# Performance work log

Hardware: AMD Instinct MI355X
Metric: run time of the kernel (lower is better)

Reference implementation:

```python
import jax, jax.numpy as jnp
import numpy as np

EMBED = 1024
HEADS = 16
HEAD_DIM = EMBED // HEADS


def setup_inputs() -> dict:
    key = jax.random.key(0)
    ks = jax.random.split(key, 5)
    s = 1.0 / np.sqrt(EMBED)
    return {
        "x": jax.random.normal(ks[0], (4, 2048, EMBED), dtype=jnp.float32),
        "W_qkv": jax.random.uniform(ks[1], (EMBED, 3 * EMBED), jnp.float32, -s, s),
        "b_qkv": jax.random.uniform(ks[2], (3 * EMBED,), jnp.float32, -s, s),
        "W_out": jax.random.uniform(ks[3], (EMBED, EMBED), jnp.float32, -s, s),
        "b_out": jax.random.uniform(ks[4], (EMBED,), jnp.float32, -s, s),
    }


def reference(x, W_qkv, b_qkv, W_out, b_out):
    B, S, E = x.shape
    qkv = x @ W_qkv + b_qkv  # [B,S,3E]
    q, k, v = jnp.split(qkv, 3, axis=-1)
    # [B,S,E] -> [B,H,S,D]
    def split_heads(t):
        return t.reshape(B, S, HEADS, HEAD_DIM).transpose(0, 2, 1, 3)
    q, k, v = split_heads(q), split_heads(k), split_heads(v)
    scale = 1.0 / jnp.sqrt(jnp.asarray(HEAD_DIM, dtype=x.dtype))
    scores = jnp.einsum("bhqd,bhkd->bhqk", q, k) * scale
    attn = jax.nn.softmax(scores, axis=-1)
    out = jnp.einsum("bhqk,bhkd->bhqd", attn, v)
    out = out.transpose(0, 2, 1, 3).reshape(B, S, E)
    return out @ W_out + b_out
```

## Files before the change

kernel.cpp:

```cpp
#include <hip/hip_runtime.h>
#include <hip/hip_bf16.h>

typedef __bf16 bf16;
typedef __bf16 bf16x8 __attribute__((ext_vector_type(8)));
typedef float f32x4 __attribute__((ext_vector_type(4)));
typedef float f32x16 __attribute__((ext_vector_type(16)));

#define EMB 1024
#define SEQ 2048
#define NH 16
#define HD 64
#define MTOK 8192

__global__ __launch_bounds__(256) void cast_f32_bf16(const float* __restrict__ in,
                                                     bf16* __restrict__ out, int n8) {
    int i = blockIdx.x * blockDim.x + threadIdx.x;
    if (i < n8) {
        const float4* p = (const float4*)in + 2 * (size_t)i;
        float4 a = p[0], b = p[1];
        bf16x8 v;
        v[0] = (bf16)a.x; v[1] = (bf16)a.y; v[2] = (bf16)a.z; v[3] = (bf16)a.w;
        v[4] = (bf16)b.x; v[5] = (bf16)b.y; v[6] = (bf16)b.z; v[7] = (bf16)b.w;
        *(bf16x8*)(out + 8 * (size_t)i) = v;
    }
}

__global__ __launch_bounds__(256) void transpose_cast(const float* __restrict__ W,
                                                      bf16* __restrict__ Wt, int K, int N) {
    __shared__ float tile[32][33];
    int n0 = blockIdx.x * 32, k0 = blockIdx.y * 32;
    int tx = threadIdx.x & 31, ty = threadIdx.x >> 5;
    #pragma unroll
    for (int i = 0; i < 32; i += 8)
        tile[ty + i][tx] = W[(size_t)(k0 + ty + i) * N + n0 + tx];
    __syncthreads();
    #pragma unroll
    for (int i = 0; i < 32; i += 8)
        Wt[(size_t)(n0 + ty + i) * K + k0 + tx] = (bf16)tile[tx][ty + i];
}

#define BM 128
#define BN 128
#define BK 64
#define LDK 72

#define QSCALE 0.1803368801111f

__global__ __launch_bounds__(256) void gemm_qkv(const bf16* __restrict__ A,
                                                const bf16* __restrict__ Bt,
                                                const float* __restrict__ bias,
                                                bf16* __restrict__ qws, bf16* __restrict__ kws,
                                                bf16* __restrict__ vt) {
    __shared__ bf16 sA[BM][LDK];
    __shared__ bf16 sB[BN][LDK];
    const int K = 1024;
    int m0 = blockIdx.x * BM, n0 = blockIdx.y * BN;
    int t = threadIdx.x, lane = t & 63, w = t >> 6;
    int wr = w >> 1, wc = w & 1;
    int l15 = lane & 15, quad = lane >> 4;

    f32x4 acc[4][4];
    #pragma unroll
    for (int i = 0; i < 4; i++)
        #pragma unroll
        for (int j = 0; j < 4; j++) acc[i][j] = (f32x4){0.f, 0.f, 0.f, 0.f};

    int srow = t >> 3, sc8 = (t & 7) * 8;
    for (int kt = 0; kt < K; kt += BK) {
        #pragma unroll
        for (int p = 0; p < 4; p++) {
            int r = srow + p * 32;
            *(uint4*)&sA[r][sc8] = *(const uint4*)(A + (size_t)(m0 + r) * K + kt + sc8);
            *(uint4*)&sB[r][sc8] = *(const uint4*)(Bt + (size_t)(n0 + r) * K + kt + sc8);
        }
        __syncthreads();
        #pragma unroll
        for (int ks = 0; ks < BK; ks += 32) {
            int kk = ks + quad * 8;
            bf16x8 af[4], bfr[4];
            #pragma unroll
            for (int mt = 0; mt < 4; mt++) af[mt] = *(const bf16x8*)&sA[wr * 64 + mt * 16 + l15][kk];
            #pragma unroll
            for (int nt = 0; nt < 4; nt++) bfr[nt] = *(const bf16x8*)&sB[wc * 64 + nt * 16 + l15][kk];
            #pragma unroll
            for (int mt = 0; mt < 4; mt++)
                #pragma unroll
                for (int nt = 0; nt < 4; nt++)
                    acc[mt][nt] = __builtin_amdgcn_mfma_f32_16x16x32_bf16(af[mt], bfr[nt], acc[mt][nt], 0, 0, 0);
        }
        __syncthreads();
    }
    #pragma unroll
    for (int mt = 0; mt < 4; mt++)
        #pragma unroll
        for (int nt = 0; nt < 4; nt++) {
            int col = n0 + wc * 64 + nt * 16 + l15;
            float bv = bias[col];
            int mat = col >> 10;
            int e = col & 1023;
            int h = e >> 6, d = e & 63;
            int row0 = m0 + wr * 64 + mt * 16 + quad * 4;
            int bb = row0 >> 11, s0 = row0 & 2047;
            int bh = bb * NH + h;
            float vv[4];
            #pragma unroll
            for (int r = 0; r < 4; r++) vv[r] = acc[mt][nt][r] + bv;
            if (mat == 0) {
                #pragma unroll
                for (int r = 0; r < 4; r++)
                    qws[((size_t)bh * SEQ + s0 + r) * HD + d] = (bf16)(vv[r] * QSCALE);
            } else if (mat == 1) {
                #pragma unroll
                for (int r = 0; r < 4; r++)
                    kws[((size_t)bh * SEQ + s0 + r) * HD + d] = (bf16)vv[r];
            } else {
                ushort4 pk;
                pk.x = __builtin_bit_cast(unsigned short, (bf16)vv[0]);
                pk.y = __builtin_bit_cast(unsigned short, (bf16)vv[1]);
                pk.z = __builtin_bit_cast(unsigned short, (bf16)vv[2]);
                pk.w = __builtin_bit_cast(unsigned short, (bf16)vv[3]);
                *(ushort4*)((unsigned short*)vt + ((size_t)bh * HD + d) * SEQ + s0) = pk;
            }
        }
}

__device__ __forceinline__ unsigned pk2(float a, float b) {
    unsigned lo = (unsigned)__builtin_bit_cast(unsigned short, (bf16)a);
    unsigned hi = (unsigned)__builtin_bit_cast(unsigned short, (bf16)b);
    return lo | (hi << 16);
}

__global__ __launch_bounds__(256) void attn(const bf16* __restrict__ qws, const bf16* __restrict__ kws,
                                            const bf16* __restrict__ vt, bf16* __restrict__ ao) {
    __shared__ bf16 sK[64][72];
    __shared__ bf16 sVt[64][72];

    int q0 = blockIdx.x * 128, bh = blockIdx.y;
    int t = threadIdx.x, lane = t & 63, w = t >> 6;
    int l31 = lane & 31, hi = lane >> 5;

    const bf16* qb = qws + (size_t)bh * SEQ * HD;
    const bf16* kb = kws + (size_t)bh * SEQ * HD;
    const bf16* vtb = vt + (size_t)bh * HD * SEQ;

    bf16x8 qf[4];
    #pragma unroll
    for (int ks = 0; ks < 4; ks++)
        qf[ks] = *(const bf16x8*)(qb + (size_t)(q0 + w * 32 + l31) * HD + ks * 16 + hi * 8);

    f32x16 o[2];
    float lsum = 0.f;
    #pragma unroll
    for (int mt = 0; mt < 2; mt++)
        #pragma unroll
        for (int r = 0; r < 16; r++) o[mt][r] = 0.f;

    int krow = t >> 3, kc8 = (t & 7) * 8;
    int vdr = t >> 2, vc16 = (t & 3) * 16;

    for (int kv0 = 0; kv0 < SEQ; kv0 += 64) {
        #pragma unroll
        for (int p = 0; p < 2; p++) {
            int r = krow + p * 32;
            *(uint4*)&sK[r][kc8] = *(const uint4*)(kb + (size_t)(kv0 + r) * HD + kc8);
        }
        {
            const bf16* src = vtb + (size_t)vdr * SEQ + kv0 + vc16;
            *(uint4*)&sVt[vdr][vc16] = *(const uint4*)src;
            *(uint4*)&sVt[vdr][vc16 + 8] = *(const uint4*)(src + 8);
        }
        __syncthreads();

        f32x16 sacc[2];
        #pragma unroll
        for (int nt = 0; nt < 2; nt++)
            #pragma unroll
            for (int r = 0; r < 16; r++) sacc[nt][r] = 0.f;
        #pragma unroll
        for (int ks = 0; ks < 4; ks++)
            #pragma unroll
            for (int nt = 0; nt < 2; nt++) {
                bf16x8 kf = *(const bf16x8*)&sK[nt * 32 + l31][ks * 16 + hi * 8];
                sacc[nt] = __builtin_amdgcn_mfma_f32_32x32x16_bf16(kf, qf[ks], sacc[nt], 0, 0, 0);
            }

        bf16x8 pb[4];
        #pragma unroll
        for (int nt = 0; nt < 2; nt++) {
            float e[16];
            #pragma unroll
            for (int r = 0; r < 16; r++) {
                e[r] = __builtin_amdgcn_exp2f(sacc[nt][r]);
                lsum += e[r];
            }
            #pragma unroll
            for (int blk = 0; blk < 2; blk++) {
                int b = blk * 8;
                unsigned a0 = pk2(e[b + 0], e[b + 1]);
                unsigned a1 = pk2(e[b + 2], e[b + 3]);
                unsigned b0 = pk2(e[b + 4], e[b + 5]);
                unsigned b1 = pk2(e[b + 6], e[b + 7]);
                asm("v_permlane32_swap_b32 %0, %1" : "+v"(a0), "+v"(b0));
                asm("v_permlane32_swap_b32 %0, %1" : "+v"(a1), "+v"(b1));
                uint4 f;
                f.x = a0; f.y = a1; f.z = b0; f.w = b1;
                pb[nt * 2 + blk] = __builtin_bit_cast(bf16x8, f);
            }
        }

        #pragma unroll
        for (int s = 0; s < 4; s++)
            #pragma unroll
            for (int mt = 0; mt < 2; mt++) {
                bf16x8 vf = *(const bf16x8*)&sVt[mt * 32 + l31][s * 16 + hi * 8];
                o[mt] = __builtin_amdgcn_mfma_f32_32x32x16_bf16(vf, pb[s], o[mt], 0, 0, 0);
            }
        __syncthreads();
    }

    float inv = __builtin_amdgcn_rcpf(lsum + __shfl_xor(lsum, 32));

    int h = bh & 15, bb = bh >> 4;
    int q = q0 + w * 32 + l31;
    #pragma unroll
    for (int mt = 0; mt < 2; mt++)
        #pragma unroll
        for (int g = 0; g < 4; g++) {
            ushort4 pk;
            pk.x = __builtin_bit_cast(unsigned short, (bf16)(o[mt][4 * g + 0] * inv));
            pk.y = __builtin_bit_cast(unsigned short, (bf16)(o[mt][4 * g + 1] * inv));
            pk.z = __builtin_bit_cast(unsigned short, (bf16)(o[mt][4 * g + 2] * inv));
            pk.w = __builtin_bit_cast(unsigned short, (bf16)(o[mt][4 * g + 3] * inv));
            *(ushort4*)((unsigned short*)ao + ((size_t)(bb * SEQ + q)) * EMB + h * HD + mt * 32 + 8 * g + 4 * hi) = pk;
        }
}

__global__ __launch_bounds__(256) void gemm_out(const bf16* __restrict__ A,
                                                const bf16* __restrict__ Bt,
                                                const float* __restrict__ bias,
                                                float* __restrict__ out) {
    __shared__ bf16 sA[BM][LDK];
    __shared__ bf16 sB[BN][LDK];
    const int K = 1024;
    int m0 = blockIdx.x * BM, n0 = blockIdx.y * BN;
    int t = threadIdx.x, lane = t & 63, w = t >> 6;
    int wr = w >> 1, wc = w & 1;
    int l15 = lane & 15, quad = lane >> 4;

    f32x4 acc[4][4];
    #pragma unroll
    for (int i = 0; i < 4; i++)
        #pragma unroll
        for (int j = 0; j < 4; j++) acc[i][j] = (f32x4){0.f, 0.f, 0.f, 0.f};

    int srow = t >> 3, sc8 = (t & 7) * 8;
    for (int kt = 0; kt < K; kt += BK) {
        #pragma unroll
        for (int p = 0; p < 4; p++) {
            int r = srow + p * 32;
            *(uint4*)&sA[r][sc8] = *(const uint4*)(A + (size_t)(m0 + r) * K + kt + sc8);
            *(uint4*)&sB[r][sc8] = *(const uint4*)(Bt + (size_t)(n0 + r) * K + kt + sc8);
        }
        __syncthreads();
        #pragma unroll
        for (int ks = 0; ks < BK; ks += 32) {
            int kk = ks + quad * 8;
            bf16x8 af[4], bfr[4];
            #pragma unroll
            for (int mt = 0; mt < 4; mt++) af[mt] = *(const bf16x8*)&sA[wr * 64 + mt * 16 + l15][kk];
            #pragma unroll
            for (int nt = 0; nt < 4; nt++) bfr[nt] = *(const bf16x8*)&sB[wc * 64 + nt * 16 + l15][kk];
            #pragma unroll
            for (int mt = 0; mt < 4; mt++)
                #pragma unroll
                for (int nt = 0; nt < 4; nt++)
                    acc[mt][nt] = __builtin_amdgcn_mfma_f32_16x16x32_bf16(af[mt], bfr[nt], acc[mt][nt], 0, 0, 0);
        }
        __syncthreads();
    }
    #pragma unroll
    for (int mt = 0; mt < 4; mt++)
        #pragma unroll
        for (int nt = 0; nt < 4; nt++) {
            int col = n0 + wc * 64 + nt * 16 + l15;
            float bv = bias[col];
            #pragma unroll
            for (int r = 0; r < 4; r++) {
                int row = m0 + wr * 64 + mt * 16 + quad * 4 + r;
                out[(size_t)row * EMB + col] = acc[mt][nt][r] + bv;
            }
        }
}

extern "C" void kernel_launch(void* const* d_in, const int* in_sizes, int n_in,
                              void* d_out, int out_size, void* d_ws, size_t ws_size,
                              hipStream_t stream) {
    const float* x     = (const float*)d_in[0];
    const float* W_qkv = (const float*)d_in[1];
    const float* b_qkv = (const float*)d_in[2];
    const float* W_out = (const float*)d_in[3];
    const float* b_out = (const float*)d_in[4];
    float* out = (float*)d_out;

    char* ws = (char*)d_ws;
    bf16* xb    = (bf16*)(ws);
    bf16* wqkvT = (bf16*)(ws + (size_t)(16 << 20));
    bf16* woutT = (bf16*)(ws + (size_t)(22 << 20));
    bf16* qws   = (bf16*)(ws + (size_t)(24 << 20));
    bf16* kws   = (bf16*)(ws + (size_t)(40 << 20));
    bf16* vt    = (bf16*)(ws + (size_t)(56 << 20));
    bf16* aow   = (bf16*)(ws + (size_t)(72 << 20));

    cast_f32_bf16<<<4096, 256, 0, stream>>>(x, xb, MTOK * EMB / 8);
    transpose_cast<<<dim3(3 * EMB / 32, EMB / 32), 256, 0, stream>>>(W_qkv, wqkvT, EMB, 3 * EMB);
    transpose_cast<<<dim3(EMB / 32, EMB / 32), 256, 0, stream>>>(W_out, woutT, EMB, EMB);
    gemm_qkv<<<dim3(MTOK / BM, 3 * EMB / BN), 256, 0, stream>>>(xb, wqkvT, b_qkv, qws, kws, vt);
    attn<<<dim3(SEQ / 128, 64), 256, 0, stream>>>(qws, kws, vt, aow);
    gemm_out<<<dim3(MTOK / BM, EMB / BN), 256, 0, stream>>>(aow, woutT, b_out, out);
}
```

Baseline: 288.4 us.

## Double-buffer K/V tiles in attention with register prefetch and MFMA priority

The attention kernel now keeps two LDS buffers for K and V^T. It loads the next tile into registers before computing on the current one and stores it to the other buffer afterwards, so global load latency overlaps the MFMA and softmax work and one barrier per iteration goes away. It also raises wave priority around the MFMA blocks and sets launch bounds to target 4 blocks per CU. In exchange it doubles LDS use and adds registers for the prefetched data, which could limit occupancy.

```diff
diff --git a/kernel.cpp b/kernel.cpp
--- a/kernel.cpp
+++ b/kernel.cpp
@@ -130,10 +130,10 @@
     return lo | (hi << 16);
 }
 
-__global__ __launch_bounds__(256) void attn(const bf16* __restrict__ qws, const bf16* __restrict__ kws,
-                                            const bf16* __restrict__ vt, bf16* __restrict__ ao) {
-    __shared__ bf16 sK[64][72];
-    __shared__ bf16 sVt[64][72];
+__global__ __launch_bounds__(256, 4) void attn(const bf16* __restrict__ qws, const bf16* __restrict__ kws,
+                                               const bf16* __restrict__ vt, bf16* __restrict__ ao) {
+    __shared__ bf16 sK[2][64][72];
+    __shared__ bf16 sVt[2][64][72];
 
     int q0 = blockIdx.x * 128, bh = blockIdx.y;
     int t = threadIdx.x, lane = t & 63, w = t >> 6;
@@ -158,31 +158,46 @@
     int krow = t >> 3, kc8 = (t & 7) * 8;
     int vdr = t >> 2, vc16 = (t & 3) * 16;
 
+    {
+        uint4 k0 = *(const uint4*)(kb + (size_t)krow * HD + kc8);
+        uint4 k1 = *(const uint4*)(kb + (size_t)(krow + 32) * HD + kc8);
+        const bf16* src = vtb + (size_t)vdr * SEQ + vc16;
+        uint4 v0 = *(const uint4*)src;
+        uint4 v1 = *(const uint4*)(src + 8);
+        *(uint4*)&sK[0][krow][kc8] = k0;
+        *(uint4*)&sK[0][krow + 32][kc8] = k1;
+        *(uint4*)&sVt[0][vdr][vc16] = v0;
+        *(uint4*)&sVt[0][vdr][vc16 + 8] = v1;
+    }
+
+    int cur = 0;
     for (int kv0 = 0; kv0 < SEQ; kv0 += 64) {
-        #pragma unroll
-        for (int p = 0; p < 2; p++) {
-            int r = krow + p * 32;
-            *(uint4*)&sK[r][kc8] = *(const uint4*)(kb + (size_t)(kv0 + r) * HD + kc8);
-        }
-        {
-            const bf16* src = vtb + (size_t)vdr * SEQ + kv0 + vc16;
-            *(uint4*)&sVt[vdr][vc16] = *(const uint4*)src;
-            *(uint4*)&sVt[vdr][vc16 + 8] = *(const uint4*)(src + 8);
-        }
-        __syncthreads();
+        __syncthreads();
+
+        int nxt = kv0 + 64;
+        uint4 nk0, nk1, nv0, nv1;
+        if (nxt < SEQ) {
+            nk0 = *(const uint4*)(kb + (size_t)(nxt + krow) * HD + kc8);
+            nk1 = *(const uint4*)(kb + (size_t)(nxt + krow + 32) * HD + kc8);
+            const bf16* src = vtb + (size_t)vdr * SEQ + nxt + vc16;
+            nv0 = *(const uint4*)src;
+            nv1 = *(const uint4*)(src + 8);
+        }
 
         f32x16 sacc[2];
         #pragma unroll
         for (int nt = 0; nt < 2; nt++)
             #pragma unroll
             for (int r = 0; r < 16; r++) sacc[nt][r] = 0.f;
+        __builtin_amdgcn_s_setprio(1);
         #pragma unroll
         for (int ks = 0; ks < 4; ks++)
             #pragma unroll
             for (int nt = 0; nt < 2; nt++) {
-                bf16x8 kf = *(const bf16x8*)&sK[nt * 32 + l31][ks * 16 + hi * 8];
+                bf16x8 kf = *(const bf16x8*)&sK[cur][nt * 32 + l31][ks * 16 + hi * 8];
                 sacc[nt] = __builtin_amdgcn_mfma_f32_32x32x16_bf16(kf, qf[ks], sacc[nt], 0, 0, 0);
             }
+        __builtin_amdgcn_s_setprio(0);
 
         bf16x8 pb[4];
         #pragma unroll
@@ -208,14 +223,23 @@
             }
         }
 
+        __builtin_amdgcn_s_setprio(1);
         #pragma unroll
         for (int s = 0; s < 4; s++)
             #pragma unroll
             for (int mt = 0; mt < 2; mt++) {
-                bf16x8 vf = *(const bf16x8*)&sVt[mt * 32 + l31][s * 16 + hi * 8];
+                bf16x8 vf = *(const bf16x8*)&sVt[cur][mt * 32 + l31][s * 16 + hi * 8];
                 o[mt] = __builtin_amdgcn_mfma_f32_32x32x16_bf16(vf, pb[s], o[mt], 0, 0, 0);
             }
-        __syncthreads();
+        __builtin_amdgcn_s_setprio(0);
+
+        if (nxt < SEQ) {
+            *(uint4*)&sK[cur ^ 1][krow][kc8] = nk0;
+            *(uint4*)&sK[cur ^ 1][krow + 32][kc8] = nk1;
+            *(uint4*)&sVt[cur ^ 1][vdr][vc16] = nv0;
+            *(uint4*)&sVt[cur ^ 1][vdr][vc16 + 8] = nv1;
+        }
+        cur ^= 1;
     }
 
     float inv = __builtin_amdgcn_rcpf(lsum + __shfl_xor(lsum, 32));
```

Measured after the change: 283.5 us. About the same (-1.7%).
